# Kernel optimization log

Hardware: AMD Instinct MI355X
Metric: run time of the kernel (lower is better)

The kernel has to match this reference:

```python
import jax, jax.numpy as jnp
import numpy as np

MAX_REL = 8  # max_relative_position
B, H, L, D = 2, 16, 2048, 64


def setup_inputs() -> dict:
    key = jax.random.key(0)
    kq, kk, kv, kb = jax.random.split(key, 4)
    return {
        "q": jax.random.normal(kq, (B, H, L, D), dtype=jnp.float32),
        "k": jax.random.normal(kk, (B, H, L, D), dtype=jnp.float32),
        "v": jax.random.normal(kv, (B, H, L, D), dtype=jnp.float32),
        "relative_bias": jax.random.normal(kb, (2 * MAX_REL + 1,), dtype=jnp.float32),
    }


def reference(q, k, v, relative_bias):
    Bq, Hq, Lq, Dq = q.shape
    scale = jnp.sqrt(jnp.asarray(Dq, dtype=q.dtype))
    # [B,H,L,L] attention scores
    scores = jnp.einsum("bhqd,bhkd->bhqk", q, k) / scale
    pos = jnp.arange(Lq)
    rel = pos[None, :] - pos[:, None]                 # [L,L] (col - row), matches torch code
    idx = jnp.clip(rel, -MAX_REL, MAX_REL) + MAX_REL  # [L,L] in [0, 2*MAX_REL]
    bias = relative_bias[idx]                         # [L,L] gather from bias table
    scores = scores + bias[None, None, :, :]
    attn = jax.nn.softmax(scores, axis=-1)
    return jnp.einsum("bhqk,bhkd->bhqd", attn, v)
```

## Files before the change

### kernel.cpp

```cpp
#include <hip/hip_runtime.h>
#include <hip/hip_bf16.h>


#define LOG2E 1.44269504088896f

constexpr int Lv = 2048, Dv = 64;
constexpr int BH  = 32;
constexpr int BQ  = 128;
constexpr int WQ  = 32;
constexpr int BKT = 64;
constexpr int NQT = Lv / BQ;
constexpr int NKT = Lv / BKT;
constexpr int LDK = 72;
constexpr int MAXREL = 8;

typedef __bf16 bf16x8 __attribute__((ext_vector_type(8)));
typedef __bf16 bf16x4 __attribute__((ext_vector_type(4)));
typedef float  f32x4  __attribute__((ext_vector_type(4)));

static __device__ __forceinline__ unsigned pack2bf(float a, float b) {
    __bf16 x = (__bf16)a, y = (__bf16)b;
    unsigned short ux = __builtin_bit_cast(unsigned short, x);
    unsigned short uy = __builtin_bit_cast(unsigned short, y);
    return (unsigned)ux | ((unsigned)uy << 16);
}

__global__ __launch_bounds__(256, 2) void relattn_kernel(
    const float* __restrict__ Q, const float* __restrict__ K,
    const float* __restrict__ V, const float* __restrict__ RB,
    float* __restrict__ O)
{
    __shared__ __align__(16) __bf16 sK[2][BKT * LDK];
    __shared__ __align__(16) __bf16 sV[2][Dv * LDK];
    __shared__ float sRB[2 * MAXREL + 1];

    const int tid  = threadIdx.x;
    const int w    = tid >> 6;
    const int lane = tid & 63;
    const int l16  = lane & 15;
    const int lg   = lane >> 4;

    const int bh = blockIdx.x & (BH - 1);
    const int qt = blockIdx.x >> 5;

    const size_t base = (size_t)bh * Lv * Dv;
    const float* Qb = Q + base + (size_t)qt * BQ * Dv;
    const float* Kb = K + base;
    const float* Vb = V + base;
    float*       Ob = O + base + (size_t)qt * BQ * Dv;

    if (tid < 2 * MAXREL + 1) sRB[tid] = RB[tid] * LOG2E;

    const float qsc = 0.125f * LOG2E;
    bf16x8 qfrag[2][2];
    #pragma unroll
    for (int h = 0; h < 2; ++h) {
        const float* qrow = Qb + (w * WQ + h * 16 + l16) * Dv;
        #pragma unroll
        for (int s = 0; s < 2; ++s) {
            const float4 a = *(const float4*)(qrow + lg * 8 + 32 * s);
            const float4 b = *(const float4*)(qrow + lg * 8 + 32 * s + 4);
            bf16x8 f;
            f[0] = (__bf16)(a.x * qsc); f[1] = (__bf16)(a.y * qsc);
            f[2] = (__bf16)(a.z * qsc); f[3] = (__bf16)(a.w * qsc);
            f[4] = (__bf16)(b.x * qsc); f[5] = (__bf16)(b.y * qsc);
            f[6] = (__bf16)(b.z * qsc); f[7] = (__bf16)(b.w * qsc);
            qfrag[h][s] = f;
        }
    }

    f32x4 oacc[2][4];
    f32x4 lacc[2];
    #pragma unroll
    for (int h = 0; h < 2; ++h) {
        lacc[h] = (f32x4){0.f, 0.f, 0.f, 0.f};
        #pragma unroll
        for (int t = 0; t < 4; ++t)
            #pragma unroll
            for (int r = 0; r < 4; ++r) oacc[h][t][r] = 0.f;
    }

    const int kr0 = tid >> 4;
    const int kc4 = (tid & 15) * 4;
    const int vkk0 = (tid & 31) * 2;
    const int vd0  = (tid >> 5) * 8;
    const int vcol = (vkk0 & 35) | ((vkk0 & 12) << 1) | ((vkk0 & 16) >> 2);

    float4 kreg[4], vreg[4];
    auto loadKV = [&](int kt) {
        const float* Ks = Kb + (size_t)kt * BKT * Dv;
        const float* Vs = Vb + (size_t)kt * BKT * Dv;
        #pragma unroll
        for (int p = 0; p < 4; ++p)
            kreg[p] = *(const float4*)(Ks + (p * 16 + kr0) * Dv + kc4);
        vreg[0] = *(const float4*)(Vs + vkk0 * Dv + vd0);
        vreg[1] = *(const float4*)(Vs + vkk0 * Dv + vd0 + 4);
        vreg[2] = *(const float4*)(Vs + (vkk0 + 1) * Dv + vd0);
        vreg[3] = *(const float4*)(Vs + (vkk0 + 1) * Dv + vd0 + 4);
    };

    loadKV(0);

    const int qw0 = qt * BQ + w * WQ;
    const int qgl = qw0 + l16;

    for (int kt = 0; kt < NKT; ++kt) {
        const int buf = kt & 1;
        #pragma unroll
        for (int p = 0; p < 4; ++p) {
            bf16x4 pk;
            pk[0] = (__bf16)kreg[p].x; pk[1] = (__bf16)kreg[p].y;
            pk[2] = (__bf16)kreg[p].z; pk[3] = (__bf16)kreg[p].w;
            *(bf16x4*)&sK[buf][(p * 16 + kr0) * LDK + kc4] = pk;
        }
        #pragma unroll
        for (int j = 0; j < 4; ++j) {
            *(unsigned*)&sV[buf][(vd0 + j) * LDK + vcol] =
                pack2bf(vreg[0][j], vreg[2][j]);
            *(unsigned*)&sV[buf][(vd0 + 4 + j) * LDK + vcol] =
                pack2bf(vreg[1][j], vreg[3][j]);
        }
        __syncthreads();

        if (kt + 1 < NKT) loadKV(kt + 1);

        f32x4 sacc[2][4];
        #pragma unroll
        for (int h = 0; h < 2; ++h)
            #pragma unroll
            for (int t = 0; t < 4; ++t)
                #pragma unroll
                for (int r = 0; r < 4; ++r) sacc[h][t][r] = 0.f;
        #pragma unroll
        for (int s = 0; s < 2; ++s) {
            #pragma unroll
            for (int t = 0; t < 4; ++t) {
                bf16x8 a = *(const bf16x8*)&sK[buf][(t * 16 + l16) * LDK + lg * 8 + 32 * s];
                sacc[0][t] = __builtin_amdgcn_mfma_f32_16x16x32_bf16(a, qfrag[0][s], sacc[0][t], 0, 0, 0);
                sacc[1][t] = __builtin_amdgcn_mfma_f32_16x16x32_bf16(a, qfrag[1][s], sacc[1][t], 0, 0, 0);
            }
        }

        const int k0 = kt * BKT;
        bf16x8 pfrag[2][2];
        #pragma unroll
        for (int h = 0; h < 2; ++h) {
            const int qw0h = qw0 + h * 16;
            if (k0 >= qw0h + 15 + MAXREL) {
                const float bc = sRB[2 * MAXREL];
                #pragma unroll
                for (int t = 0; t < 4; ++t)
                    #pragma unroll
                    for (int r = 0; r < 4; ++r) {
                        float p = __builtin_amdgcn_exp2f(sacc[h][t][r] + bc);
                        lacc[h][r] += p;
                        pfrag[h][t >> 1][(t & 1) * 4 + r] = (__bf16)p;
                    }
            } else if (k0 + BKT - 1 + MAXREL <= qw0h) {
                const float bc = sRB[0];
                #pragma unroll
                for (int t = 0; t < 4; ++t)
                    #pragma unroll
                    for (int r = 0; r < 4; ++r) {
                        float p = __builtin_amdgcn_exp2f(sacc[h][t][r] + bc);
                        lacc[h][r] += p;
                        pfrag[h][t >> 1][(t & 1) * 4 + r] = (__bf16)p;
                    }
            } else {
                const int kkb = k0 + lg * 4 - (qgl + h * 16);
                #pragma unroll
                for (int t = 0; t < 4; ++t) {
                    #pragma unroll
                    for (int r = 0; r < 4; ++r) {
                        int d = kkb + t * 16 + r;
                        d = d < -MAXREL ? -MAXREL : (d > MAXREL ? MAXREL : d);
                        float p = __builtin_amdgcn_exp2f(sacc[h][t][r] + sRB[d + MAXREL]);
                        lacc[h][r] += p;
                        pfrag[h][t >> 1][(t & 1) * 4 + r] = (__bf16)p;
                    }
                }
            }
        }

        #pragma unroll
        for (int s = 0; s < 2; ++s) {
            #pragma unroll
            for (int t = 0; t < 4; ++t) {
                bf16x8 vf = *(const bf16x8*)&sV[buf][(t * 16 + l16) * LDK + lg * 8 + 32 * s];
                oacc[0][t] = __builtin_amdgcn_mfma_f32_16x16x32_bf16(vf, pfrag[0][s], oacc[0][t], 0, 0, 0);
                oacc[1][t] = __builtin_amdgcn_mfma_f32_16x16x32_bf16(vf, pfrag[1][s], oacc[1][t], 0, 0, 0);
            }
        }
    }

    #pragma unroll
    for (int h = 0; h < 2; ++h) {
        float l = lacc[h][0] + lacc[h][1] + lacc[h][2] + lacc[h][3];
        l += __shfl_xor(l, 16);
        l += __shfl_xor(l, 32);
        const float linv = 1.f / l;
        float* orow = Ob + (w * WQ + h * 16 + l16) * Dv;
        #pragma unroll
        for (int t = 0; t < 4; ++t) {
            float4 o;
            o.x = oacc[h][t][0] * linv; o.y = oacc[h][t][1] * linv;
            o.z = oacc[h][t][2] * linv; o.w = oacc[h][t][3] * linv;
            *(float4*)(orow + t * 16 + lg * 4) = o;
        }
    }
}

extern "C" void kernel_launch(void* const* d_in, const int* in_sizes, int n_in,
                              void* d_out, int out_size, void* d_ws, size_t ws_size,
                              hipStream_t stream) {
    const float* q  = (const float*)d_in[0];
    const float* k  = (const float*)d_in[1];
    const float* v  = (const float*)d_in[2];
    const float* rb = (const float*)d_in[3];
    float* out = (float*)d_out;
    relattn_kernel<<<dim3(BH * NQT), dim3(256), 0, stream>>>(q, k, v, rb, out);
}
```

Measured before the change: 136.0 us.

## Split each key tile across wave pairs and merge partial outputs via LDS

Doubles the block to 512 threads with 8 waves, where each pair of waves shares the same 32 query rows and splits each 64-key tile into two halves. Each wave computes scores, softmax numerators and the PV product for its half, and at the end one wave writes its partial output and row sum to shared memory for its partner to add and normalise. The next K/V tile prefetch is now issued before the barrier. This halves per-wave register state and raises waves per CU to hide latency, at the cost of a final shared-memory reduction and extra synchronisation.

```diff
diff --git a/kernel.cpp b/kernel.cpp
--- a/kernel.cpp
+++ b/kernel.cpp
@@ -7,11 +7,11 @@
 constexpr int Lv = 2048, Dv = 64;
 constexpr int BH  = 32;
 constexpr int BQ  = 128;
-constexpr int WQ  = 32;
 constexpr int BKT = 64;
 constexpr int NQT = Lv / BQ;
 constexpr int NKT = Lv / BKT;
 constexpr int LDK = 72;
+constexpr int LDO = 68;
 constexpr int MAXREL = 8;
 
 typedef __bf16 bf16x8 __attribute__((ext_vector_type(8)));
@@ -25,20 +25,25 @@
     return (unsigned)ux | ((unsigned)uy << 16);
 }
 
-__global__ __launch_bounds__(256, 2) void relattn_kernel(
+__global__ __launch_bounds__(512, 4) void relattn_kernel(
     const float* __restrict__ Q, const float* __restrict__ K,
     const float* __restrict__ V, const float* __restrict__ RB,
     float* __restrict__ O)
 {
-    __shared__ __align__(16) __bf16 sK[2][BKT * LDK];
-    __shared__ __align__(16) __bf16 sV[2][Dv * LDK];
+    constexpr int SKBYTES = 2 * BKT * LDK * 2;
+    constexpr int SVBYTES = 2 * Dv  * LDK * 2;
+    __shared__ __align__(16) unsigned char smem[SKBYTES + SVBYTES];
     __shared__ float sRB[2 * MAXREL + 1];
+    __bf16* sK = (__bf16*)smem;
+    __bf16* sV = (__bf16*)(smem + SKBYTES);
 
     const int tid  = threadIdx.x;
     const int w    = tid >> 6;
     const int lane = tid & 63;
     const int l16  = lane & 15;
     const int lg   = lane >> 4;
+    const int pair = w >> 1;
+    const int wh   = w & 1;
 
     const int bh = blockIdx.x & (BH - 1);
     const int qt = blockIdx.x >> 5;
@@ -55,7 +60,7 @@
     bf16x8 qfrag[2][2];
     #pragma unroll
     for (int h = 0; h < 2; ++h) {
-        const float* qrow = Qb + (w * WQ + h * 16 + l16) * Dv;
+        const float* qrow = Qb + (pair * 32 + h * 16 + l16) * Dv;
         #pragma unroll
         for (int s = 0; s < 2; ++s) {
             const float4 a = *(const float4*)(qrow + lg * 8 + 32 * s);
@@ -83,129 +88,148 @@
     const int kr0 = tid >> 4;
     const int kc4 = (tid & 15) * 4;
     const int vkk0 = (tid & 31) * 2;
-    const int vd0  = (tid >> 5) * 8;
+    const int vd0  = (tid >> 5) * 4;
     const int vcol = (vkk0 & 35) | ((vkk0 & 12) << 1) | ((vkk0 & 16) >> 2);
 
-    float4 kreg[4], vreg[4];
+    float4 kreg[2], vreg[2];
     auto loadKV = [&](int kt) {
         const float* Ks = Kb + (size_t)kt * BKT * Dv;
         const float* Vs = Vb + (size_t)kt * BKT * Dv;
-        #pragma unroll
-        for (int p = 0; p < 4; ++p)
-            kreg[p] = *(const float4*)(Ks + (p * 16 + kr0) * Dv + kc4);
+        kreg[0] = *(const float4*)(Ks + kr0 * Dv + kc4);
+        kreg[1] = *(const float4*)(Ks + (32 + kr0) * Dv + kc4);
         vreg[0] = *(const float4*)(Vs + vkk0 * Dv + vd0);
-        vreg[1] = *(const float4*)(Vs + vkk0 * Dv + vd0 + 4);
-        vreg[2] = *(const float4*)(Vs + (vkk0 + 1) * Dv + vd0);
-        vreg[3] = *(const float4*)(Vs + (vkk0 + 1) * Dv + vd0 + 4);
+        vreg[1] = *(const float4*)(Vs + (vkk0 + 1) * Dv + vd0);
     };
 
     loadKV(0);
 
-    const int qw0 = qt * BQ + w * WQ;
+    const int qw0 = qt * BQ + pair * 32;
     const int qgl = qw0 + l16;
 
     for (int kt = 0; kt < NKT; ++kt) {
         const int buf = kt & 1;
-        #pragma unroll
-        for (int p = 0; p < 4; ++p) {
+        __bf16* sKb = sK + buf * (BKT * LDK);
+        __bf16* sVb = sV + buf * (Dv * LDK);
+
+        #pragma unroll
+        for (int p = 0; p < 2; ++p) {
             bf16x4 pk;
             pk[0] = (__bf16)kreg[p].x; pk[1] = (__bf16)kreg[p].y;
             pk[2] = (__bf16)kreg[p].z; pk[3] = (__bf16)kreg[p].w;
-            *(bf16x4*)&sK[buf][(p * 16 + kr0) * LDK + kc4] = pk;
+            *(bf16x4*)&sKb[(p * 32 + kr0) * LDK + kc4] = pk;
         }
         #pragma unroll
         for (int j = 0; j < 4; ++j) {
-            *(unsigned*)&sV[buf][(vd0 + j) * LDK + vcol] =
-                pack2bf(vreg[0][j], vreg[2][j]);
-            *(unsigned*)&sV[buf][(vd0 + 4 + j) * LDK + vcol] =
-                pack2bf(vreg[1][j], vreg[3][j]);
-        }
+            *(unsigned*)&sVb[(vd0 + j) * LDK + vcol] =
+                pack2bf(vreg[0][j], vreg[1][j]);
+        }
+        if (kt + 1 < NKT) loadKV(kt + 1);
         __syncthreads();
 
-        if (kt + 1 < NKT) loadKV(kt + 1);
-
-        f32x4 sacc[2][4];
+        f32x4 sacc[2][2];
         #pragma unroll
         for (int h = 0; h < 2; ++h)
             #pragma unroll
-            for (int t = 0; t < 4; ++t)
-                #pragma unroll
-                for (int r = 0; r < 4; ++r) sacc[h][t][r] = 0.f;
+            for (int tl = 0; tl < 2; ++tl)
+                #pragma unroll
+                for (int r = 0; r < 4; ++r) sacc[h][tl][r] = 0.f;
         #pragma unroll
         for (int s = 0; s < 2; ++s) {
             #pragma unroll
-            for (int t = 0; t < 4; ++t) {
-                bf16x8 a = *(const bf16x8*)&sK[buf][(t * 16 + l16) * LDK + lg * 8 + 32 * s];
-                sacc[0][t] = __builtin_amdgcn_mfma_f32_16x16x32_bf16(a, qfrag[0][s], sacc[0][t], 0, 0, 0);
-                sacc[1][t] = __builtin_amdgcn_mfma_f32_16x16x32_bf16(a, qfrag[1][s], sacc[1][t], 0, 0, 0);
+            for (int tl = 0; tl < 2; ++tl) {
+                bf16x8 a = *(const bf16x8*)&sKb[((2 * wh + tl) * 16 + l16) * LDK + lg * 8 + 32 * s];
+                sacc[0][tl] = __builtin_amdgcn_mfma_f32_16x16x32_bf16(a, qfrag[0][s], sacc[0][tl], 0, 0, 0);
+                sacc[1][tl] = __builtin_amdgcn_mfma_f32_16x16x32_bf16(a, qfrag[1][s], sacc[1][tl], 0, 0, 0);
             }
         }
 
-        const int k0 = kt * BKT;
-        bf16x8 pfrag[2][2];
+        const int k0 = kt * BKT + wh * 32;
+        bf16x8 pfrag[2];
         #pragma unroll
         for (int h = 0; h < 2; ++h) {
-            const int qw0h = qw0 + h * 16;
-            if (k0 >= qw0h + 15 + MAXREL) {
+            const int qlo = qw0 + h * 16;
+            if (k0 >= qlo + 15 + MAXREL) {
                 const float bc = sRB[2 * MAXREL];
                 #pragma unroll
-                for (int t = 0; t < 4; ++t)
+                for (int tl = 0; tl < 2; ++tl)
                     #pragma unroll
                     for (int r = 0; r < 4; ++r) {
-                        float p = __builtin_amdgcn_exp2f(sacc[h][t][r] + bc);
+                        float p = __builtin_amdgcn_exp2f(sacc[h][tl][r] + bc);
                         lacc[h][r] += p;
-                        pfrag[h][t >> 1][(t & 1) * 4 + r] = (__bf16)p;
+                        pfrag[h][tl * 4 + r] = (__bf16)p;
                     }
-            } else if (k0 + BKT - 1 + MAXREL <= qw0h) {
+            } else if (k0 + 31 + MAXREL <= qlo) {
                 const float bc = sRB[0];
                 #pragma unroll
-                for (int t = 0; t < 4; ++t)
+                for (int tl = 0; tl < 2; ++tl)
                     #pragma unroll
                     for (int r = 0; r < 4; ++r) {
-                        float p = __builtin_amdgcn_exp2f(sacc[h][t][r] + bc);
+                        float p = __builtin_amdgcn_exp2f(sacc[h][tl][r] + bc);
                         lacc[h][r] += p;
-                        pfrag[h][t >> 1][(t & 1) * 4 + r] = (__bf16)p;
+                        pfrag[h][tl * 4 + r] = (__bf16)p;
                     }
             } else {
                 const int kkb = k0 + lg * 4 - (qgl + h * 16);
                 #pragma unroll
-                for (int t = 0; t < 4; ++t) {
+                for (int tl = 0; tl < 2; ++tl) {
                     #pragma unroll
                     for (int r = 0; r < 4; ++r) {
-                        int d = kkb + t * 16 + r;
+                        int d = kkb + tl * 16 + r;
                         d = d < -MAXREL ? -MAXREL : (d > MAXREL ? MAXREL : d);
-                        float p = __builtin_amdgcn_exp2f(sacc[h][t][r] + sRB[d + MAXREL]);
+                        float p = __builtin_amdgcn_exp2f(sacc[h][tl][r] + sRB[d + MAXREL]);
                         lacc[h][r] += p;
-                        pfrag[h][t >> 1][(t & 1) * 4 + r] = (__bf16)p;
+                        pfrag[h][tl * 4 + r] = (__bf16)p;
                     }
                 }
             }
         }
 
         #pragma unroll
-        for (int s = 0; s < 2; ++s) {
-            #pragma unroll
-            for (int t = 0; t < 4; ++t) {
-                bf16x8 vf = *(const bf16x8*)&sV[buf][(t * 16 + l16) * LDK + lg * 8 + 32 * s];
-                oacc[0][t] = __builtin_amdgcn_mfma_f32_16x16x32_bf16(vf, pfrag[0][s], oacc[0][t], 0, 0, 0);
-                oacc[1][t] = __builtin_amdgcn_mfma_f32_16x16x32_bf16(vf, pfrag[1][s], oacc[1][t], 0, 0, 0);
-            }
-        }
-    }
-
+        for (int t = 0; t < 4; ++t) {
+            bf16x8 vf = *(const bf16x8*)&sVb[(t * 16 + l16) * LDK + lg * 8 + 32 * wh];
+            oacc[0][t] = __builtin_amdgcn_mfma_f32_16x16x32_bf16(vf, pfrag[0], oacc[0][t], 0, 0, 0);
+            oacc[1][t] = __builtin_amdgcn_mfma_f32_16x16x32_bf16(vf, pfrag[1], oacc[1][t], 0, 0, 0);
+        }
+    }
+
+    float lh[2];
     #pragma unroll
     for (int h = 0; h < 2; ++h) {
         float l = lacc[h][0] + lacc[h][1] + lacc[h][2] + lacc[h][3];
         l += __shfl_xor(l, 16);
         l += __shfl_xor(l, 32);
-        const float linv = 1.f / l;
-        float* orow = Ob + (w * WQ + h * 16 + l16) * Dv;
-        #pragma unroll
-        for (int t = 0; t < 4; ++t) {
-            float4 o;
-            o.x = oacc[h][t][0] * linv; o.y = oacc[h][t][1] * linv;
-            o.z = oacc[h][t][2] * linv; o.w = oacc[h][t][3] * linv;
-            *(float4*)(orow + t * 16 + lg * 4) = o;
+        lh[h] = l;
+    }
+
+    __syncthreads();
+    float* sO = (float*)smem;
+    float* sL = (float*)(smem + 4 * 32 * LDO * 4);
+    if (wh == 1) {
+        #pragma unroll
+        for (int h = 0; h < 2; ++h) {
+            #pragma unroll
+            for (int t = 0; t < 4; ++t)
+                *(f32x4*)&sO[(pair * 32 + h * 16 + l16) * LDO + t * 16 + lg * 4] = oacc[h][t];
+            if (lg == 0) sL[pair * 32 + h * 16 + l16] = lh[h];
+        }
+    }
+    __syncthreads();
+    if (wh == 0) {
+        #pragma unroll
+        for (int h = 0; h < 2; ++h) {
+            const float lt = lh[h] + sL[pair * 32 + h * 16 + l16];
+            const float linv = 1.f / lt;
+            float* orow = Ob + (pair * 32 + h * 16 + l16) * Dv;
+            #pragma unroll
+            for (int t = 0; t < 4; ++t) {
+                f32x4 oo = *(const f32x4*)&sO[(pair * 32 + h * 16 + l16) * LDO + t * 16 + lg * 4];
+                float4 o;
+                o.x = (oacc[h][t][0] + oo[0]) * linv;
+                o.y = (oacc[h][t][1] + oo[1]) * linv;
+                o.z = (oacc[h][t][2] + oo[2]) * linv;
+                o.w = (oacc[h][t][3] + oo[3]) * linv;
+                *(float4*)(orow + t * 16 + lg * 4) = o;
+            }
         }
     }
 }
@@ -218,5 +242,5 @@
     const float* v  = (const float*)d_in[2];
     const float* rb = (const float*)d_in[3];
     float* out = (float*)d_out;
-    relattn_kernel<<<dim3(BH * NQT), dim3(256), 0, stream>>>(q, k, v, rb, out);
+    relattn_kernel<<<dim3(BH * NQT), dim3(512), 0, stream>>>(q, k, v, rb, out);
 }
```

Result: slower. 148.5 us (+9.2%).
